# Optimization experiments

Measured on AMD Instinct MI355X. Metric: run time of the kernel, lower is better.

Reference implementation:

```python
import jax, jax.numpy as jnp
import numpy as np

V, L, H, E, S = 50257, 12, 12, 768, 1024
B, T = 4, 1024
D = E // H
EPS = 1e-5


def setup_inputs() -> dict:
    key = jax.random.key(0)
    ks = jax.random.split(key, 16)
    n = lambda k, shape: (jax.random.normal(k, shape, dtype=jnp.float32) * 0.02)
    return {
        'idx': jax.random.randint(ks[0], (B, T), 0, V),
        'wte': n(ks[1], (V, E)),
        'wpe': n(ks[2], (S, E)),
        'ln1_g': jnp.ones((L, E)), 'ln1_b': jnp.zeros((L, E)),
        'attn_w': n(ks[3], (L, E, 3 * E)), 'attn_b': jnp.zeros((L, 3 * E)),
        'proj_w': n(ks[4], (L, E, E)), 'proj_b': jnp.zeros((L, E)),
        'ln2_g': jnp.ones((L, E)), 'ln2_b': jnp.zeros((L, E)),
        'fc_w': n(ks[5], (L, E, 4 * E)), 'fc_b': jnp.zeros((L, 4 * E)),
        'mproj_w': n(ks[6], (L, 4 * E, E)), 'mproj_b': jnp.zeros((L, E)),
        'lnf_g': jnp.ones((E,)), 'lnf_b': jnp.zeros((E,)),
    }


def layer_norm(x, g, b):
    m = jnp.mean(x, axis=-1, keepdims=True)
    v = jnp.var(x, axis=-1, keepdims=True)
    return (x - m) * jax.lax.rsqrt(v + EPS) * g + b


def reference(idx, wte, wpe, ln1_g, ln1_b, attn_w, attn_b, proj_w, proj_b,
              ln2_g, ln2_b, fc_w, fc_b, mproj_w, mproj_b, lnf_g, lnf_b):
    b, t = idx.shape
    x = wte[idx] + wpe[:t]  # [B,T,E]
    causal = jnp.tril(jnp.ones((t, t), dtype=bool))
    neg_inf = jnp.finfo(x.dtype).min
    for l in range(L):
        h = layer_norm(x, ln1_g[l], ln1_b[l])
        qkv = h @ attn_w[l] + attn_b[l]  # [B,T,3E]
        q, k, v = jnp.split(qkv, 3, axis=-1)
        q = q.reshape(b, t, H, D).transpose(0, 2, 1, 3)  # [B,H,T,D]
        k = k.reshape(b, t, H, D).transpose(0, 2, 1, 3)
        v = v.reshape(b, t, H, D).transpose(0, 2, 1, 3)
        att = jnp.einsum('bhqd,bhkd->bhqk', q, k) / jnp.sqrt(jnp.float32(D))
        att = jnp.where(causal, att, neg_inf)
        att = jax.nn.softmax(att, axis=-1)
        y = jnp.einsum('bhqk,bhkd->bhqd', att, v)
        y = y.transpose(0, 2, 1, 3).reshape(b, t, E)
        x = x + y @ proj_w[l] + proj_b[l]
        h2 = layer_norm(x, ln2_g[l], ln2_b[l])
        h2 = jax.nn.gelu(h2 @ fc_w[l] + fc_b[l], approximate=True)
        x = x + h2 @ mproj_w[l] + mproj_b[l]
    x = layer_norm(x, lnf_g, lnf_b)
    logits = x @ wte.T  # tied lm_head
    return logits
```

## Files before the change

### kernel.cpp

```cpp
#include <hip/hip_runtime.h>
#include <hip/hip_bf16.h>
#include <math.h>

#define VSZ 50257
#define VPAD2 50432
#define NLAYER 12
#define NH 12
#define EMB 768
#define TSEQ 1024
#define NB 4
#define MROWS (NB * TSEQ)
#define DHEAD 64
#define LN_EPS 1e-5f

typedef __attribute__((ext_vector_type(8))) short bf16x8;
typedef __attribute__((ext_vector_type(4))) float f32x4;

__device__ __forceinline__ void load_lds16(const void* g, void* l) {
    __builtin_amdgcn_global_load_lds((const __attribute__((address_space(1))) unsigned int*)g,
                                     (__attribute__((address_space(3))) unsigned int*)l,
                                     16, 0, 0);
}

__global__ void embed_kernel(const int* __restrict__ idx, const float* __restrict__ wte,
                             const float* __restrict__ wpe, float* __restrict__ x) {
    int row = blockIdx.x;
    int t = row & (TSEQ - 1);
    int tok = idx[row];
    const float* wt = wte + (size_t)tok * EMB;
    const float* wp = wpe + (size_t)t * EMB;
    float* xo = x + (size_t)row * EMB;
    for (int e = threadIdx.x; e < EMB; e += blockDim.x)
        xo[e] = wt[e] + wp[e];
}

__global__ void ln_kernel(const float* __restrict__ x, const float* __restrict__ g,
                          const float* __restrict__ b, __hip_bfloat16* __restrict__ out) {
    int row = blockIdx.x;
    const float* xr = x + (size_t)row * EMB;
    __hip_bfloat16* yr = out + (size_t)row * EMB;
    int tid = threadIdx.x;
    float v0 = xr[tid], v1 = xr[tid + 256], v2 = xr[tid + 512];
    float s = v0 + v1 + v2;
    float ss = v0 * v0 + v1 * v1 + v2 * v2;
    #pragma unroll
    for (int i = 1; i < 64; i <<= 1) {
        s  += __shfl_xor(s, i, 64);
        ss += __shfl_xor(ss, i, 64);
    }
    __shared__ float sm[4], sv[4];
    int lane = tid & 63, wid = tid >> 6;
    if (lane == 0) { sm[wid] = s; sv[wid] = ss; }
    __syncthreads();
    float sum = sm[0] + sm[1] + sm[2] + sm[3];
    float sqs = sv[0] + sv[1] + sv[2] + sv[3];
    float mean = sum * (1.0f / EMB);
    float var = sqs * (1.0f / EMB) - mean * mean;
    float rstd = rsqrtf(var + LN_EPS);
    yr[tid]       = __float2bfloat16((v0 - mean) * rstd * g[tid]       + b[tid]);
    yr[tid + 256] = __float2bfloat16((v1 - mean) * rstd * g[tid + 256] + b[tid + 256]);
    yr[tid + 512] = __float2bfloat16((v2 - mean) * rstd * g[tid + 512] + b[tid + 512]);
}

__global__ void convT4_kernel(const float* __restrict__ aw, const float* __restrict__ pw,
                              const float* __restrict__ fw, const float* __restrict__ mw,
                              __hip_bfloat16* __restrict__ awT, __hip_bfloat16* __restrict__ pwT,
                              __hip_bfloat16* __restrict__ fwT, __hip_bfloat16* __restrict__ mwT) {
    __shared__ float tile[32][33];
    int bid = blockIdx.x;
    const float* W; __hip_bfloat16* Wt; int K, N, t;
    if (bid < 1728)      { W = aw; Wt = awT; K = 768;  N = 2304; t = bid; }
    else if (bid < 2304) { W = pw; Wt = pwT; K = 768;  N = 768;  t = bid - 1728; }
    else if (bid < 4608) { W = fw; Wt = fwT; K = 768;  N = 3072; t = bid - 2304; }
    else                 { W = mw; Wt = mwT; K = 3072; N = 768;  t = bid - 4608; }
    int NT = N >> 5;
    int n0 = (t % NT) << 5, k0 = (t / NT) << 5;
    int tx = threadIdx.x & 31, ty = threadIdx.x >> 5;
    #pragma unroll
    for (int i = ty; i < 32; i += 8)
        tile[i][tx] = W[(size_t)(k0 + i) * N + n0 + tx];
    __syncthreads();
    #pragma unroll
    for (int i = ty; i < 32; i += 8)
        Wt[(size_t)(n0 + i) * K + k0 + tx] = __float2bfloat16(tile[tx][i]);
}

__global__ void conv_wte_kernel(const float* __restrict__ wte, __hip_bfloat16* __restrict__ o) {
    int row = blockIdx.x;
    bool pad = row >= VSZ;
    const float* src = wte + (size_t)row * EMB;
    __hip_bfloat16* dst = o + (size_t)row * EMB;
    for (int e = threadIdx.x; e < EMB; e += blockDim.x)
        dst[e] = __float2bfloat16(pad ? 0.0f : src[e]);
}

template <bool GELU, bool RES, int OUT>
__global__ __launch_bounds__(512) void gemm_bt(
                        const __hip_bfloat16* __restrict__ A, const __hip_bfloat16* __restrict__ B,
                        const float* __restrict__ bias, const float* __restrict__ res,
                        float* __restrict__ Cf, __hip_bfloat16* __restrict__ Cb,
                        __hip_bfloat16* __restrict__ vt,
                        int K, int ldc, int Nclip) {
    __shared__ __hip_bfloat16 Ash[128 * 64];
    __shared__ __hip_bfloat16 Bsh[128 * 64];
    const int tid = threadIdx.x;
    const int lane = tid & 63, wid = tid >> 6;
    const int wr = wid >> 2, wc = wid & 3;

    const int nwg = gridDim.x;
    const int NT = nwg >> 5;
    const int cpx = nwg >> 3;
    const int wg = (blockIdx.x & 7) * cpx + (blockIdx.x >> 3);
    const int bandsz = NT << 3;
    const int band = wg / bandsz;
    const int rem = wg - band * bandsz;
    const int m0 = (band * 8 + (rem & 7)) * 128;
    const int n0 = (rem >> 3) * 128;

    f32x4 acc[4][2] = {};
    const int srow = lane >> 3;
    const int scol = ((lane & 7) ^ srow) * 8;

    const int lr16 = lane & 15;
    const int hi = lane >> 4;

    for (int k0 = 0; k0 < K; k0 += 64) {
        #pragma unroll
        for (int it = 0; it < 2; ++it) {
            int c = wid + it * 8;
            const __hip_bfloat16* ga = A + (size_t)(m0 + c * 8 + srow) * K + k0 + scol;
            load_lds16(ga, &Ash[c * 512]);
            const __hip_bfloat16* gb = B + (size_t)(n0 + c * 8 + srow) * K + k0 + scol;
            load_lds16(gb, &Bsh[c * 512]);
        }
        __syncthreads();
        bf16x8 a[4][2], b[2][2];
        #pragma unroll
        for (int m = 0; m < 4; ++m)
            #pragma unroll
            for (int kk = 0; kk < 2; ++kk) {
                int ra = wr * 64 + m * 16 + lr16;
                int ca = (kk * 32 + hi * 8) ^ ((ra & 7) * 8);
                a[m][kk] = *(const bf16x8*)&Ash[ra * 64 + ca];
            }
        #pragma unroll
        for (int n = 0; n < 2; ++n)
            #pragma unroll
            for (int kk = 0; kk < 2; ++kk) {
                int rb = wc * 32 + n * 16 + lr16;
                int cb = (kk * 32 + hi * 8) ^ ((rb & 7) * 8);
                b[n][kk] = *(const bf16x8*)&Bsh[rb * 64 + cb];
            }
        #pragma unroll
        for (int kk = 0; kk < 2; ++kk)
            #pragma unroll
            for (int m = 0; m < 4; ++m)
                #pragma unroll
                for (int n = 0; n < 2; ++n)
                    acc[m][n] = __builtin_amdgcn_mfma_f32_16x16x32_bf16(a[m][kk], b[n][kk], acc[m][n], 0, 0, 0);
        __syncthreads();
    }

    const int crow0 = m0 + wr * 64, ccol0 = n0 + wc * 32;
    #pragma unroll
    for (int m = 0; m < 4; ++m) {
        #pragma unroll
        for (int n = 0; n < 2; ++n) {
            int col = ccol0 + n * 16 + lr16;
            if (col >= Nclip) continue;
            float bv = bias ? bias[col] : 0.0f;
            #pragma unroll
            for (int j = 0; j < 4; ++j) {
                int r = crow0 + m * 16 + hi * 4 + j;
                float v = acc[m][n][j] + bv;
                if (GELU) {
                    float t = 0.7978845608028654f * (v + 0.044715f * v * v * v);
                    v = 0.5f * v * (1.0f + tanhf(t));
                }
                if (RES) v += res[(size_t)r * ldc + col];
                if (OUT == 0) Cf[(size_t)r * ldc + col] = v;
                else if (OUT == 1) Cb[(size_t)r * ldc + col] = __float2bfloat16(v);
                else {
                    if (col < 2 * EMB) Cb[(size_t)r * (2 * EMB) + col] = __float2bfloat16(v);
                    else {
                        int hh = (col - 2 * EMB) >> 6, dd = (col - 2 * EMB) & 63;
                        int bb = r >> 10, tt = r & 1023;
                        vt[(((size_t)bb * NH + hh) * 64 + dd) * TSEQ + tt] = __float2bfloat16(v);
                    }
                }
            }
        }
    }
}

#define G256_STAGE_A(KT, MH, P) do { \
    int ktw_ = (KT) % 12; \
    load_lds16(A + (size_t)(m0 + (MH) * 64 + srow) * 768 + ktw_ * 64 + sgr8, \
               &lds[(P) * 2][(MH) * 8192 + wid * 512]); \
    load_lds16(A + (size_t)(m0 + 128 + (MH) * 64 + srow) * 768 + ktw_ * 64 + sgr8, \
               &lds[(P) * 2][(MH) * 8192 + 4096 + wid * 512]); \
} while (0)

#define G256_STAGE_B(KT, NH, P) do { \
    int ktw_ = (KT) % 12; \
    load_lds16(Bm + (size_t)(bwc0 * 64 + (NH) * 32 + brow) * 768 + ktw_ * 64 + sgr8, \
               &lds[(P) * 2 + 1][(NH) * 8192 + wid * 512]); \
    load_lds16(Bm + (size_t)((2 + bwc0) * 64 + (NH) * 32 + brow) * 768 + ktw_ * 64 + sgr8, \
               &lds[(P) * 2 + 1][(NH) * 8192 + 4096 + wid * 512]); \
} while (0)

#define G256_PHASE(MH, NH, P, STAGE_STMT, VM) do { \
    bf16x8 af[4][2], bf[2][2]; \
    _Pragma("unroll") \
    for (int f = 0; f < 4; ++f) \
        _Pragma("unroll") \
        for (int kk = 0; kk < 2; ++kk) { \
            int pr = (MH) * 128 + wr * 64 + f * 16 + lr16; \
            af[f][kk] = *(const bf16x8*)((const char*)lds[(P) * 2] + pr * 128 + ((kk * 64 + hi * 16) ^ ((lr16 & 7) << 4))); \
        } \
    _Pragma("unroll") \
    for (int nn = 0; nn < 2; ++nn) \
        _Pragma("unroll") \
        for (int kk = 0; kk < 2; ++kk) { \
            int pr = (NH) * 128 + wc * 32 + nn * 16 + lr16; \
            bf[nn][kk] = *(const bf16x8*)((const char*)lds[(P) * 2 + 1] + pr * 128 + ((kk * 64 + hi * 16) ^ ((lr16 & 7) << 4))); \
        } \
    STAGE_STMT; \
    asm volatile("s_waitcnt vmcnt(" #VM ")" ::: "memory"); \
    __builtin_amdgcn_s_barrier(); \
    asm volatile("s_waitcnt lgkmcnt(0)" ::: "memory"); \
    __builtin_amdgcn_sched_barrier(0); \
    __builtin_amdgcn_s_setprio(1); \
    _Pragma("unroll") \
    for (int kk = 0; kk < 2; ++kk) \
        _Pragma("unroll") \
        for (int f = 0; f < 4; ++f) \
            _Pragma("unroll") \
            for (int nn = 0; nn < 2; ++nn) \
                acc[(MH) * 4 + f][(NH) * 2 + nn] = __builtin_amdgcn_mfma_f32_16x16x32_bf16( \
                    af[f][kk], bf[nn][kk], acc[(MH) * 4 + f][(NH) * 2 + nn], 0, 0, 0); \
    __builtin_amdgcn_s_setprio(0); \
    __builtin_amdgcn_s_barrier(); \
} while (0)

__global__ __launch_bounds__(512, 1) void gemm256(const __hip_bfloat16* __restrict__ A,
                                                  const __hip_bfloat16* __restrict__ Bw,
                                                  float* __restrict__ C) {
    __shared__ __hip_bfloat16 lds[4][16384];
    const int tid = threadIdx.x;
    const int lane = tid & 63, wid = tid >> 6;
    const int wr = wid >> 2, wc = wid & 3;
    const int lr16 = lane & 15, hi = lane >> 4;

    const int bid = blockIdx.x;
    const int wg = (bid & 7) * 394 + (bid >> 3);
    const int band = wg / 1576, rem = wg % 1576;
    const int mt = band * 8 + (rem & 7), nt = rem >> 3;
    const size_t m0 = (size_t)mt * 256;
    const __hip_bfloat16* Bm = Bw + (size_t)nt * 256 * 768;

    const int srow = tid >> 3;
    const int sgr8 = ((tid & 7) ^ ((tid >> 3) & 7)) * 8;
    const int brow = (tid >> 3) & 31;
    const int bwc0 = tid >> 8;

    f32x4 acc[8][4] = {};

    G256_STAGE_A(0, 0, 0);
    G256_STAGE_B(0, 0, 0);
    G256_STAGE_A(0, 1, 0);
    G256_STAGE_B(0, 1, 0);
    G256_STAGE_A(1, 0, 1);
    G256_STAGE_B(1, 0, 1);
    asm volatile("s_waitcnt vmcnt(8)" ::: "memory");
    __builtin_amdgcn_s_barrier();

    for (int kt2 = 0; kt2 < 12; kt2 += 2) {
        G256_PHASE(0, 0, 0, G256_STAGE_A(kt2 + 1, 1, 1), 6);
        G256_PHASE(0, 1, 0, G256_STAGE_B(kt2 + 1, 1, 1), 10);
        G256_PHASE(1, 0, 0, G256_STAGE_A(kt2 + 2, 0, 0), 10);
        G256_PHASE(1, 1, 0, G256_STAGE_B(kt2 + 2, 0, 0), 8);
        G256_PHASE(0, 0, 1, G256_STAGE_A(kt2 + 2, 1, 0), 6);
        G256_PHASE(0, 1, 1, G256_STAGE_B(kt2 + 2, 1, 0), 10);
        G256_PHASE(1, 0, 1, G256_STAGE_A(kt2 + 3, 0, 1), 10);
        G256_PHASE(1, 1, 1, G256_STAGE_B(kt2 + 3, 0, 1), 8);
    }

    const int ccol0 = nt * 256 + wc * 64;
    #pragma unroll
    for (int mf = 0; mf < 8; ++mf) {
        size_t row = m0 + wr * 128 + (mf >> 2) * 64 + (mf & 3) * 16 + hi * 4;
        #pragma unroll
        for (int nf = 0; nf < 4; ++nf) {
            int col = ccol0 + nf * 16 + lr16;
            if (col < VSZ) {
                #pragma unroll
                for (int j = 0; j < 4; ++j)
                    C[(row + j) * VSZ + col] = acc[mf][nf][j];
            }
        }
    }
}

__global__ __launch_bounds__(256) void flash_attn(const __hip_bfloat16* __restrict__ qk,
                                                  const __hip_bfloat16* __restrict__ vT,
                                                  __hip_bfloat16* __restrict__ y) {
    const int qt = blockIdx.x, h = blockIdx.y, b = blockIdx.z;
    const int tid = threadIdx.x;
    const int lane = tid & 63, w = tid >> 6;
    const int g = lane >> 4, lr = lane & 15;

    __shared__ char KshB[64 * 128];
    __shared__ char VshB[64 * 128];
    __shared__ char PshB[4][16 * 128];

    const __hip_bfloat16* qrow = qk + ((size_t)(b * TSEQ + qt * 64 + w * 16 + lr)) * 1536 + h * 64;
    bf16x8 qf0 = *(const bf16x8*)(qrow + g * 8);
    bf16x8 qf1 = *(const bf16x8*)(qrow + 32 + g * 8);

    float m[4], l[4];
    f32x4 o[4];
    #pragma unroll
    for (int j = 0; j < 4; ++j) { m[j] = -1e30f; l[j] = 0.0f; }
    #pragma unroll
    for (int n = 0; n < 4; ++n) o[n] = (f32x4){0.f, 0.f, 0.f, 0.f};

    const int r0 = tid >> 3;
    const int c0 = (tid & 7) * 8;

    for (int kt = 0; kt <= qt; ++kt) {
        __syncthreads();
        #pragma unroll
        for (int it = 0; it < 2; ++it) {
            int r = r0 + it * 32;
            bf16x8 kv = *(const bf16x8*)(qk + ((size_t)(b * TSEQ + kt * 64 + r)) * 1536 + EMB + h * 64 + c0);
            *(bf16x8*)(KshB + ((r * 128 + c0 * 2) ^ ((r & 7) << 4))) = kv;
            bf16x8 vv = *(const bf16x8*)(vT + (((size_t)(b * NH + h)) * 64 + r) * TSEQ + kt * 64 + c0);
            *(bf16x8*)(VshB + ((r * 128 + c0 * 2) ^ ((r & 7) << 4))) = vv;
        }
        __syncthreads();

        f32x4 s[4] = {};
        #pragma unroll
        for (int n = 0; n < 4; ++n) {
            int kr = n * 16 + lr;
            bf16x8 kb0 = *(const bf16x8*)(KshB + ((kr * 128 + g * 16) ^ ((kr & 7) << 4)));
            bf16x8 kb1 = *(const bf16x8*)(KshB + ((kr * 128 + 64 + g * 16) ^ ((kr & 7) << 4)));
            s[n] = __builtin_amdgcn_mfma_f32_16x16x32_bf16(qf0, kb0, s[n], 0, 0, 0);
            s[n] = __builtin_amdgcn_mfma_f32_16x16x32_bf16(qf1, kb1, s[n], 0, 0, 0);
        }

        const bool diag = (kt == qt);
        float tmax[4] = {-1e30f, -1e30f, -1e30f, -1e30f};
        #pragma unroll
        for (int n = 0; n < 4; ++n)
            #pragma unroll
            for (int j = 0; j < 4; ++j) {
                float v = s[n][j] * 0.125f;
                if (diag && (n * 16 + lr > w * 16 + g * 4 + j)) v = -1e30f;
                s[n][j] = v;
                tmax[j] = fmaxf(tmax[j], v);
            }
        #pragma unroll
        for (int j = 0; j < 4; ++j)
            #pragma unroll
            for (int i = 1; i < 16; i <<= 1)
                tmax[j] = fmaxf(tmax[j], __shfl_xor(tmax[j], i, 64));

        float lsum[4] = {0.f, 0.f, 0.f, 0.f};
        float pexp[4][4];
        #pragma unroll
        for (int j = 0; j < 4; ++j) {
            float mn = fmaxf(m[j], tmax[j]);
            float sc = __expf(m[j] - mn);
            l[j] *= sc;
            m[j] = mn;
            #pragma unroll
            for (int n = 0; n < 4; ++n) {
                float p = __expf(s[n][j] - mn);
                pexp[n][j] = p;
                lsum[j] += p;
                o[n][j] *= sc;
            }
        }
        #pragma unroll
        for (int j = 0; j < 4; ++j) {
            #pragma unroll
            for (int i = 1; i < 16; i <<= 1) lsum[j] += __shfl_xor(lsum[j], i, 64);
            l[j] += lsum[j];
        }

        char* P = PshB[w];
        #pragma unroll
        for (int n = 0; n < 4; ++n)
            #pragma unroll
            for (int j = 0; j < 4; ++j) {
                int rw = g * 4 + j;
                *(__hip_bfloat16*)(P + ((rw * 128 + (n * 16 + lr) * 2) ^ ((rw & 7) << 4))) =
                    __float2bfloat16(pexp[n][j]);
            }
        asm volatile("s_waitcnt lgkmcnt(0)" ::: "memory");
        bf16x8 pa0 = *(const bf16x8*)(P + ((lr * 128 + g * 16) ^ ((lr & 7) << 4)));
        bf16x8 pa1 = *(const bf16x8*)(P + ((lr * 128 + 64 + g * 16) ^ ((lr & 7) << 4)));
        #pragma unroll
        for (int n = 0; n < 4; ++n) {
            int vr = n * 16 + lr;
            bf16x8 vb0 = *(const bf16x8*)(VshB + ((vr * 128 + g * 16) ^ ((vr & 7) << 4)));
            bf16x8 vb1 = *(const bf16x8*)(VshB + ((vr * 128 + 64 + g * 16) ^ ((vr & 7) << 4)));
            o[n] = __builtin_amdgcn_mfma_f32_16x16x32_bf16(pa0, vb0, o[n], 0, 0, 0);
            o[n] = __builtin_amdgcn_mfma_f32_16x16x32_bf16(pa1, vb1, o[n], 0, 0, 0);
        }
    }

    #pragma unroll
    for (int j = 0; j < 4; ++j) {
        float inv = 1.0f / l[j];
        int row = b * TSEQ + qt * 64 + w * 16 + g * 4 + j;
        #pragma unroll
        for (int n = 0; n < 4; ++n)
            y[(size_t)row * EMB + h * 64 + n * 16 + lr] = __float2bfloat16(o[n][j] * inv);
    }
}

extern "C" void kernel_launch(void* const* d_in, const int* in_sizes, int n_in,
                              void* d_out, int out_size, void* d_ws, size_t ws_size,
                              hipStream_t stream) {
    const int*   idx     = (const int*)d_in[0];
    const float* wte     = (const float*)d_in[1];
    const float* wpe     = (const float*)d_in[2];
    const float* ln1_g   = (const float*)d_in[3];
    const float* ln1_b   = (const float*)d_in[4];
    const float* attn_w  = (const float*)d_in[5];
    const float* attn_b  = (const float*)d_in[6];
    const float* proj_w  = (const float*)d_in[7];
    const float* proj_b  = (const float*)d_in[8];
    const float* ln2_g   = (const float*)d_in[9];
    const float* ln2_b   = (const float*)d_in[10];
    const float* fc_w    = (const float*)d_in[11];
    const float* fc_b    = (const float*)d_in[12];
    const float* mproj_w = (const float*)d_in[13];
    const float* mproj_b = (const float*)d_in[14];
    const float* lnf_g   = (const float*)d_in[15];
    const float* lnf_b   = (const float*)d_in[16];
    float* out = (float*)d_out;

    char* w = (char*)d_ws;
    float* x = (float*)w;                      w += (size_t)MROWS * EMB * 4;
    __hip_bfloat16* qkb = (__hip_bfloat16*)w;  w += (size_t)MROWS * 2 * EMB * 2;
    __hip_bfloat16* vTb = (__hip_bfloat16*)w;  w += (size_t)NB * NH * 64 * TSEQ * 2;
    __hip_bfloat16* h = (__hip_bfloat16*)w;    w += (size_t)MROWS * EMB * 2;
    __hip_bfloat16* y = (__hip_bfloat16*)w;    w += (size_t)MROWS * EMB * 2;
    __hip_bfloat16* g = (__hip_bfloat16*)w;    w += (size_t)MROWS * 4 * EMB * 2;
    __hip_bfloat16* wqkvT = (__hip_bfloat16*)w;   w += (size_t)3 * EMB * EMB * 2;
    __hip_bfloat16* wprojT = (__hip_bfloat16*)w;  w += (size_t)EMB * EMB * 2;
    __hip_bfloat16* wfcT = (__hip_bfloat16*)w;    w += (size_t)4 * EMB * EMB * 2;
    __hip_bfloat16* wmprojT = (__hip_bfloat16*)w; w += (size_t)4 * EMB * EMB * 2;
    __hip_bfloat16* wteB = (__hip_bfloat16*)w;    w += (size_t)VPAD2 * EMB * 2;

    dim3 blk256(256), blk512(512);

    embed_kernel<<<MROWS, blk256, 0, stream>>>(idx, wte, wpe, x);
    conv_wte_kernel<<<VPAD2, blk256, 0, stream>>>(wte, wteB);

    for (int l = 0; l < NLAYER; l++) {
        const float* aw = attn_w + (size_t)l * EMB * 3 * EMB;
        const float* ab = attn_b + (size_t)l * 3 * EMB;
        const float* pw = proj_w + (size_t)l * EMB * EMB;
        const float* pb = proj_b + (size_t)l * EMB;
        const float* fw = fc_w   + (size_t)l * EMB * 4 * EMB;
        const float* fb = fc_b   + (size_t)l * 4 * EMB;
        const float* mw = mproj_w + (size_t)l * 4 * EMB * EMB;
        const float* mb = mproj_b + (size_t)l * EMB;

        ln_kernel<<<MROWS, blk256, 0, stream>>>(x, ln1_g + l * EMB, ln1_b + l * EMB, h);
        convT4_kernel<<<6912, blk256, 0, stream>>>(aw, pw, fw, mw, wqkvT, wprojT, wfcT, wmprojT);

        gemm_bt<false, false, 2><<<dim3((3 * EMB / 128) * 32), blk512, 0, stream>>>(
            h, wqkvT, ab, nullptr, nullptr, qkb, vTb, EMB, 3 * EMB, 3 * EMB);

        flash_attn<<<dim3(TSEQ / 64, NH, NB), blk256, 0, stream>>>(qkb, vTb, y);

        gemm_bt<false, true, 0><<<dim3((EMB / 128) * 32), blk512, 0, stream>>>(
            y, wprojT, pb, x, x, nullptr, nullptr, EMB, EMB, EMB);

        ln_kernel<<<MROWS, blk256, 0, stream>>>(x, ln2_g + l * EMB, ln2_b + l * EMB, h);

        gemm_bt<true, false, 1><<<dim3((4 * EMB / 128) * 32), blk512, 0, stream>>>(
            h, wfcT, fb, nullptr, nullptr, g, nullptr, EMB, 4 * EMB, 4 * EMB);

        gemm_bt<false, true, 0><<<dim3((EMB / 128) * 32), blk512, 0, stream>>>(
            g, wmprojT, mb, x, x, nullptr, nullptr, 4 * EMB, EMB, EMB);
    }

    ln_kernel<<<MROWS, blk256, 0, stream>>>(x, lnf_g, lnf_b, h);

    gemm256<<<dim3((VPAD2 / 256) * (MROWS / 256)), dim3(512), 0, stream>>>(h, wteB, out);
}
```

Before: 3.027 ms.

## Split-K the N=768 projection GEMMs and fuse the residual add into LayerNorm

The attention-projection and MLP-down-projection GEMMs (N=768) now use a two-way split-K. This doubles the workgroup count from 192 to 384 so more of the GPU's compute units have work. Each K half writes an fp32 partial to its own buffer, and only the first half adds the bias. A new ln_acc kernel sums the residual with both partials, writes the result back to x, and applies LayerNorm in the same pass. The cost is two extra fp32 activation buffers and more global memory traffic for writing and rereading the partials.

```diff
diff --git a/kernel.cpp b/kernel.cpp
--- a/kernel.cpp
+++ b/kernel.cpp
@@ -41,6 +41,41 @@
     __hip_bfloat16* yr = out + (size_t)row * EMB;
     int tid = threadIdx.x;
     float v0 = xr[tid], v1 = xr[tid + 256], v2 = xr[tid + 512];
+    float s = v0 + v1 + v2;
+    float ss = v0 * v0 + v1 * v1 + v2 * v2;
+    #pragma unroll
+    for (int i = 1; i < 64; i <<= 1) {
+        s  += __shfl_xor(s, i, 64);
+        ss += __shfl_xor(ss, i, 64);
+    }
+    __shared__ float sm[4], sv[4];
+    int lane = tid & 63, wid = tid >> 6;
+    if (lane == 0) { sm[wid] = s; sv[wid] = ss; }
+    __syncthreads();
+    float sum = sm[0] + sm[1] + sm[2] + sm[3];
+    float sqs = sv[0] + sv[1] + sv[2] + sv[3];
+    float mean = sum * (1.0f / EMB);
+    float var = sqs * (1.0f / EMB) - mean * mean;
+    float rstd = rsqrtf(var + LN_EPS);
+    yr[tid]       = __float2bfloat16((v0 - mean) * rstd * g[tid]       + b[tid]);
+    yr[tid + 256] = __float2bfloat16((v1 - mean) * rstd * g[tid + 256] + b[tid + 256]);
+    yr[tid + 512] = __float2bfloat16((v2 - mean) * rstd * g[tid + 512] + b[tid + 512]);
+}
+
+__global__ void ln_acc_kernel(float* __restrict__ x, const float* __restrict__ p0,
+                              const float* __restrict__ p1,
+                              const float* __restrict__ g, const float* __restrict__ b,
+                              __hip_bfloat16* __restrict__ out) {
+    int row = blockIdx.x;
+    float* xr = x + (size_t)row * EMB;
+    const float* q0 = p0 + (size_t)row * EMB;
+    const float* q1 = p1 + (size_t)row * EMB;
+    __hip_bfloat16* yr = out + (size_t)row * EMB;
+    int tid = threadIdx.x;
+    float v0 = xr[tid]       + q0[tid]       + q1[tid];
+    float v1 = xr[tid + 256] + q0[tid + 256] + q1[tid + 256];
+    float v2 = xr[tid + 512] + q0[tid + 512] + q1[tid + 512];
+    xr[tid] = v0; xr[tid + 256] = v1; xr[tid + 512] = v2;
     float s = v0 + v1 + v2;
     float ss = v0 * v0 + v1 * v1 + v2 * v2;
     #pragma unroll
@@ -94,28 +129,31 @@
         dst[e] = __float2bfloat16(pad ? 0.0f : src[e]);
 }
 
-template <bool GELU, bool RES, int OUT>
+template <bool GELU, bool RES, int OUT, bool SPLITK>
 __global__ __launch_bounds__(512) void gemm_bt(
                         const __hip_bfloat16* __restrict__ A, const __hip_bfloat16* __restrict__ B,
                         const float* __restrict__ bias, const float* __restrict__ res,
                         float* __restrict__ Cf, __hip_bfloat16* __restrict__ Cb,
-                        __hip_bfloat16* __restrict__ vt,
-                        int K, int ldc, int Nclip) {
+                        __hip_bfloat16* __restrict__ vt, float* __restrict__ Cp1,
+                        int Kc, int lda, int ldc, int Nclip) {
     __shared__ __hip_bfloat16 Ash[128 * 64];
     __shared__ __hip_bfloat16 Bsh[128 * 64];
     const int tid = threadIdx.x;
     const int lane = tid & 63, wid = tid >> 6;
     const int wr = wid >> 2, wc = wid & 3;
 
-    const int nwg = gridDim.x;
+    const int nwg_all = gridDim.x;
+    const int cpx = nwg_all >> 3;
+    int wg = (blockIdx.x & 7) * cpx + (blockIdx.x >> 3);
+    int chunk = 0, nwg = nwg_all;
+    if (SPLITK) { chunk = wg & 1; wg >>= 1; nwg = nwg_all >> 1; }
     const int NT = nwg >> 5;
-    const int cpx = nwg >> 3;
-    const int wg = (blockIdx.x & 7) * cpx + (blockIdx.x >> 3);
     const int bandsz = NT << 3;
     const int band = wg / bandsz;
     const int rem = wg - band * bandsz;
     const int m0 = (band * 8 + (rem & 7)) * 128;
     const int n0 = (rem >> 3) * 128;
+    const int koff = SPLITK ? chunk * Kc : 0;
 
     f32x4 acc[4][2] = {};
     const int srow = lane >> 3;
@@ -124,13 +162,13 @@
     const int lr16 = lane & 15;
     const int hi = lane >> 4;
 
-    for (int k0 = 0; k0 < K; k0 += 64) {
+    for (int k0 = 0; k0 < Kc; k0 += 64) {
         #pragma unroll
         for (int it = 0; it < 2; ++it) {
             int c = wid + it * 8;
-            const __hip_bfloat16* ga = A + (size_t)(m0 + c * 8 + srow) * K + k0 + scol;
+            const __hip_bfloat16* ga = A + (size_t)(m0 + c * 8 + srow) * lda + koff + k0 + scol;
             load_lds16(ga, &Ash[c * 512]);
-            const __hip_bfloat16* gb = B + (size_t)(n0 + c * 8 + srow) * K + k0 + scol;
+            const __hip_bfloat16* gb = B + (size_t)(n0 + c * 8 + srow) * lda + koff + k0 + scol;
             load_lds16(gb, &Bsh[c * 512]);
         }
         __syncthreads();
@@ -161,6 +199,8 @@
         __syncthreads();
     }
 
+    float* Co = (SPLITK && chunk) ? Cp1 : Cf;
+    const bool dobias = bias && (!SPLITK || chunk == 0);
     const int crow0 = m0 + wr * 64, ccol0 = n0 + wc * 32;
     #pragma unroll
     for (int m = 0; m < 4; ++m) {
@@ -168,7 +208,7 @@
         for (int n = 0; n < 2; ++n) {
             int col = ccol0 + n * 16 + lr16;
             if (col >= Nclip) continue;
-            float bv = bias ? bias[col] : 0.0f;
+            float bv = dobias ? bias[col] : 0.0f;
             #pragma unroll
             for (int j = 0; j < 4; ++j) {
                 int r = crow0 + m * 16 + hi * 4 + j;
@@ -178,7 +218,7 @@
                     v = 0.5f * v * (1.0f + tanhf(t));
                 }
                 if (RES) v += res[(size_t)r * ldc + col];
-                if (OUT == 0) Cf[(size_t)r * ldc + col] = v;
+                if (OUT == 0) Co[(size_t)r * ldc + col] = v;
                 else if (OUT == 1) Cb[(size_t)r * ldc + col] = __float2bfloat16(v);
                 else {
                     if (col < 2 * EMB) Cb[(size_t)r * (2 * EMB) + col] = __float2bfloat16(v);
@@ -446,6 +486,8 @@
 
     char* w = (char*)d_ws;
     float* x = (float*)w;                      w += (size_t)MROWS * EMB * 4;
+    float* p0 = (float*)w;                     w += (size_t)MROWS * EMB * 4;
+    float* p1 = (float*)w;                     w += (size_t)MROWS * EMB * 4;
     __hip_bfloat16* qkb = (__hip_bfloat16*)w;  w += (size_t)MROWS * 2 * EMB * 2;
     __hip_bfloat16* vTb = (__hip_bfloat16*)w;  w += (size_t)NB * NH * 64 * TSEQ * 2;
     __hip_bfloat16* h = (__hip_bfloat16*)w;    w += (size_t)MROWS * EMB * 2;
@@ -472,27 +514,31 @@
         const float* mw = mproj_w + (size_t)l * 4 * EMB * EMB;
         const float* mb = mproj_b + (size_t)l * EMB;
 
-        ln_kernel<<<MROWS, blk256, 0, stream>>>(x, ln1_g + l * EMB, ln1_b + l * EMB, h);
+        if (l == 0)
+            ln_kernel<<<MROWS, blk256, 0, stream>>>(x, ln1_g + l * EMB, ln1_b + l * EMB, h);
+        else
+            ln_acc_kernel<<<MROWS, blk256, 0, stream>>>(x, p0, p1, ln1_g + l * EMB, ln1_b + l * EMB, h);
+
         convT4_kernel<<<6912, blk256, 0, stream>>>(aw, pw, fw, mw, wqkvT, wprojT, wfcT, wmprojT);
 
-        gemm_bt<false, false, 2><<<dim3((3 * EMB / 128) * 32), blk512, 0, stream>>>(
-            h, wqkvT, ab, nullptr, nullptr, qkb, vTb, EMB, 3 * EMB, 3 * EMB);
+        gemm_bt<false, false, 2, false><<<dim3((3 * EMB / 128) * 32), blk512, 0, stream>>>(
+            h, wqkvT, ab, nullptr, nullptr, qkb, vTb, nullptr, EMB, EMB, 3 * EMB, 3 * EMB);
 
         flash_attn<<<dim3(TSEQ / 64, NH, NB), blk256, 0, stream>>>(qkb, vTb, y);
 
-        gemm_bt<false, true, 0><<<dim3((EMB / 128) * 32), blk512, 0, stream>>>(
-            y, wprojT, pb, x, x, nullptr, nullptr, EMB, EMB, EMB);
-
-        ln_kernel<<<MROWS, blk256, 0, stream>>>(x, ln2_g + l * EMB, ln2_b + l * EMB, h);
-
-        gemm_bt<true, false, 1><<<dim3((4 * EMB / 128) * 32), blk512, 0, stream>>>(
-            h, wfcT, fb, nullptr, nullptr, g, nullptr, EMB, 4 * EMB, 4 * EMB);
-
-        gemm_bt<false, true, 0><<<dim3((EMB / 128) * 32), blk512, 0, stream>>>(
-            g, wmprojT, mb, x, x, nullptr, nullptr, 4 * EMB, EMB, EMB);
-    }
-
-    ln_kernel<<<MROWS, blk256, 0, stream>>>(x, lnf_g, lnf_b, h);
+        gemm_bt<false, false, 0, true><<<dim3((EMB / 128) * 32 * 2), blk512, 0, stream>>>(
+            y, wprojT, pb, nullptr, p0, nullptr, nullptr, p1, EMB / 2, EMB, EMB, EMB);
+
+        ln_acc_kernel<<<MROWS, blk256, 0, stream>>>(x, p0, p1, ln2_g + l * EMB, ln2_b + l * EMB, h);
+
+        gemm_bt<true, false, 1, false><<<dim3((4 * EMB / 128) * 32), blk512, 0, stream>>>(
+            h, wfcT, fb, nullptr, nullptr, g, nullptr, nullptr, EMB, EMB, 4 * EMB, 4 * EMB);
+
+        gemm_bt<false, false, 0, true><<<dim3((EMB / 128) * 32 * 2), blk512, 0, stream>>>(
+            g, wmprojT, mb, nullptr, p0, nullptr, nullptr, p1, 2 * EMB, 4 * EMB, EMB, EMB);
+    }
+
+    ln_acc_kernel<<<MROWS, blk256, 0, stream>>>(x, p0, p1, lnf_g, lnf_b, h);
 
     gemm256<<<dim3((VPAD2 / 256) * (MROWS / 256)), dim3(512), 0, stream>>>(h, wteB, out);
 }
```

Result: faster. 2.828 ms (-6.6%).
